# Optimization experiments

Hardware: AMD Instinct MI355X
Metric: run time of the kernel (lower is better)

## Reference

```python
import jax, jax.numpy as jnp
import numpy as np

B, T = 64, 500000

def setup_inputs() -> dict:
    key = jax.random.key(0)
    k1, k2 = jax.random.split(key)
    input_attenuation = jax.random.normal(k1, (B, T), dtype=jnp.float32)
    input_wet_dry = jax.random.randint(k2, (B, T), 0, 2).astype(jnp.bool_)
    return {"input_attenuation": input_attenuation, "input_wet_dry": input_wet_dry}

def reference(input_attenuation, input_wet_dry):
    # baseline[i] = baseline[i-1] if wet[i] else attenuation[i]; baseline[0] = attenuation[0].
    # Equivalent to gathering attenuation at the most recent 'dry' index (index 0 forced dry).
    Bn, Tn = input_attenuation.shape
    t = jnp.arange(Tn, dtype=jnp.int32)
    dry = jnp.logical_not(input_wet_dry).at[:, 0].set(True)  # timestep 0 always uses attenuation[0]
    pos = jnp.where(dry, t[None, :], jnp.int32(-1))          # [B, T]
    idx = jax.lax.associative_scan(jnp.maximum, pos, axis=1)  # running max = last dry index
    return jnp.take_along_axis(input_attenuation, idx, axis=1)
```

## Files before the change

### kernel.cpp

```cpp
#include <hip/hip_runtime.h>


constexpr int WSEG   = 4096;
constexpr int WCHUNK = 256;
constexpr int WITERS = WSEG / WCHUNK;

__global__ __launch_bounds__(256) void ffill_wave_kernel(
    const float* __restrict__ att,
    const int* __restrict__ wet,
    float* __restrict__ out,
    int T, int segsPerRow)
{
    const int lane = threadIdx.x & 63;
    const int wid  = threadIdx.x >> 6;
    const int s    = blockIdx.x * 4 + wid;
    if (s >= segsPerRow) return;
    const int r    = blockIdx.y;
    const long long rowBase = (long long)r * T;
    const int base = s * WSEG;

    float carry = 0.0f;
    int hi = base;
    while (hi > 0) {
        const int start = (hi >= 64) ? (hi - 64) : 0;
        const int idx   = start + lane;
        bool dry = false;
        if (idx < hi) dry = (wet[rowBase + idx] == 0) || (idx == 0);
        const unsigned long long m = __ballot(dry);
        if (m != 0ull) {
            const int src = 63 - __clzll(m);
            carry = att[rowBase + start + src];
            break;
        }
        hi = start;
    }

    int e = base + lane * 4;
    bool valid = (e < T);
    float4 a = make_float4(0.f, 0.f, 0.f, 0.f);
    int4  wv = make_int4(1, 1, 1, 1);
    if (valid) {
        a  = *reinterpret_cast<const float4*>(att + rowBase + e);
        wv = *reinterpret_cast<const int4*>(wet + rowBase + e);
    }

    for (int it = 0; it < WITERS; ++it) {
        float4 a_n = make_float4(0.f, 0.f, 0.f, 0.f);
        int4  wv_n = make_int4(1, 1, 1, 1);
        bool valid_n = false;
        if (it + 1 < WITERS) {
            const int en = e + WCHUNK;
            valid_n = (en < T);
            if (valid_n) {
                a_n  = *reinterpret_cast<const float4*>(att + rowBase + en);
                wv_n = *reinterpret_cast<const int4*>(wet + rowBase + en);
            }
        }

        bool d0 = (wv.x == 0) || (e == 0);
        bool d1 = (wv.y == 0);
        bool d2 = (wv.z == 0);
        bool d3 = (wv.w == 0);
        if (!valid) { d0 = d1 = d2 = d3 = false; }

        const bool has = d0 | d1 | d2 | d3;
        const float lastval = d3 ? a.w : (d2 ? a.z : (d1 ? a.y : a.x));

        const unsigned long long mask = __ballot(has);
        const unsigned long long pm = mask & ((1ull << lane) - 1ull);
        const int psrc = (pm != 0ull) ? (63 - __clzll(pm)) : 0;
        const float pval = __shfl(lastval, psrc);
        const float carry_in = (pm != 0ull) ? pval : carry;

        if (valid) {
            float running = carry_in;
            float4 o;
            running = d0 ? a.x : running;  o.x = running;
            running = d1 ? a.y : running;  o.y = running;
            running = d2 ? a.z : running;  o.z = running;
            running = d3 ? a.w : running;  o.w = running;
            *reinterpret_cast<float4*>(out + rowBase + e) = o;
        }

        const int wsrc = (mask != 0ull) ? (63 - __clzll(mask)) : 0;
        const float wval = __shfl(lastval, wsrc);
        if (mask != 0ull) carry = wval;

        a = a_n; wv = wv_n; valid = valid_n; e += WCHUNK;
    }
}

extern "C" void kernel_launch(void* const* d_in, const int* in_sizes, int n_in,
                              void* d_out, int out_size, void* d_ws, size_t ws_size,
                              hipStream_t stream) {
    const float* att = (const float*)d_in[0];
    const int* wet   = (const int*)d_in[1];
    float* out       = (float*)d_out;

    const int B = 64;
    const int T = in_sizes[0] / B;
    const int segsPerRow = (T + WSEG - 1) / WSEG;
    const int blocksX = (segsPerRow + 3) / 4;

    dim3 grid(blocksX, B);
    dim3 block(256);
    ffill_wave_kernel<<<grid, block, 0, stream>>>(att, wet, out, T, segsPerRow);
}
```

Before: 308.0 us.

## Batch-prefetch four chunks per iteration, enlarge segments, use nontemporal stores

The forward-fill loop now loads four 256-element chunks at once and prefetches the next batch of four, instead of one chunk ahead. This raises the number of memory requests in flight per wave. The segment length doubles to 8192, halving the redundant backward carry searches but also halving the number of waves. Outputs are written with nontemporal stores, and the carry is simplified to a shuffle from lane 63. The larger batches raise register pressure.

```diff
diff --git a/kernel.cpp b/kernel.cpp
--- a/kernel.cpp
+++ b/kernel.cpp
@@ -1,9 +1,13 @@
 #include <hip/hip_runtime.h>
 
 
-constexpr int WSEG   = 4096;
+constexpr int BATCH  = 4;
 constexpr int WCHUNK = 256;
-constexpr int WITERS = WSEG / WCHUNK;
+constexpr int OBLK   = BATCH * WCHUNK;
+constexpr int WSEG   = 8192;
+constexpr int OUTER  = WSEG / OBLK;
+
+typedef float f4v __attribute__((ext_vector_type(4)));
 
 __global__ __launch_bounds__(256) void ffill_wave_kernel(
     const float* __restrict__ att,
@@ -28,65 +32,80 @@
         if (idx < hi) dry = (wet[rowBase + idx] == 0) || (idx == 0);
         const unsigned long long m = __ballot(dry);
         if (m != 0ull) {
-            const int src = 63 - __clzll(m);
-            carry = att[rowBase + start + src];
+            carry = att[rowBase + start + (63 - __clzll(m))];
             break;
         }
         hi = start;
     }
 
-    int e = base + lane * 4;
-    bool valid = (e < T);
-    float4 a = make_float4(0.f, 0.f, 0.f, 0.f);
-    int4  wv = make_int4(1, 1, 1, 1);
-    if (valid) {
-        a  = *reinterpret_cast<const float4*>(att + rowBase + e);
-        wv = *reinterpret_cast<const int4*>(wet + rowBase + e);
+    float4 aC[BATCH]; int4 wC[BATCH];
+    const int e0 = base + lane * 4;
+    #pragma unroll
+    for (int k = 0; k < BATCH; ++k) {
+        const int e = e0 + k * WCHUNK;
+        if (e < T) {
+            aC[k] = *reinterpret_cast<const float4*>(att + rowBase + e);
+            wC[k] = *reinterpret_cast<const int4*>(wet + rowBase + e);
+        } else {
+            aC[k] = make_float4(0.f, 0.f, 0.f, 0.f);
+            wC[k] = make_int4(1, 1, 1, 1);
+        }
     }
 
-    for (int it = 0; it < WITERS; ++it) {
-        float4 a_n = make_float4(0.f, 0.f, 0.f, 0.f);
-        int4  wv_n = make_int4(1, 1, 1, 1);
-        bool valid_n = false;
-        if (it + 1 < WITERS) {
-            const int en = e + WCHUNK;
-            valid_n = (en < T);
-            if (valid_n) {
-                a_n  = *reinterpret_cast<const float4*>(att + rowBase + en);
-                wv_n = *reinterpret_cast<const int4*>(wet + rowBase + en);
+    for (int ot = 0; ot < OUTER; ++ot) {
+        float4 aN[BATCH]; int4 wN[BATCH];
+        #pragma unroll
+        for (int k = 0; k < BATCH; ++k) {
+            aN[k] = make_float4(0.f, 0.f, 0.f, 0.f);
+            wN[k] = make_int4(1, 1, 1, 1);
+        }
+        if (ot + 1 < OUTER) {
+            const int eb = e0 + (ot + 1) * OBLK;
+            #pragma unroll
+            for (int k = 0; k < BATCH; ++k) {
+                const int e = eb + k * WCHUNK;
+                if (e < T) {
+                    aN[k] = *reinterpret_cast<const float4*>(att + rowBase + e);
+                    wN[k] = *reinterpret_cast<const int4*>(wet + rowBase + e);
+                }
             }
         }
 
-        bool d0 = (wv.x == 0) || (e == 0);
-        bool d1 = (wv.y == 0);
-        bool d2 = (wv.z == 0);
-        bool d3 = (wv.w == 0);
-        if (!valid) { d0 = d1 = d2 = d3 = false; }
+        #pragma unroll
+        for (int k = 0; k < BATCH; ++k) {
+            const int e = e0 + ot * OBLK + k * WCHUNK;
+            const bool valid = (e < T);
 
-        const bool has = d0 | d1 | d2 | d3;
-        const float lastval = d3 ? a.w : (d2 ? a.z : (d1 ? a.y : a.x));
+            bool d0 = (wC[k].x == 0) || (e == 0);
+            bool d1 = (wC[k].y == 0);
+            bool d2 = (wC[k].z == 0);
+            bool d3 = (wC[k].w == 0);
+            if (!valid) { d0 = d1 = d2 = d3 = false; }
 
-        const unsigned long long mask = __ballot(has);
-        const unsigned long long pm = mask & ((1ull << lane) - 1ull);
-        const int psrc = (pm != 0ull) ? (63 - __clzll(pm)) : 0;
-        const float pval = __shfl(lastval, psrc);
-        const float carry_in = (pm != 0ull) ? pval : carry;
+            const bool has = d0 | d1 | d2 | d3;
+            const float lastval = d3 ? aC[k].w : (d2 ? aC[k].z : (d1 ? aC[k].y : aC[k].x));
 
-        if (valid) {
+            const unsigned long long mask = __ballot(has);
+            const unsigned long long pm = mask & ((1ull << lane) - 1ull);
+            const int psrc = (pm != 0ull) ? (63 - __clzll(pm)) : 0;
+            const float pval = __shfl(lastval, psrc);
+            const float carry_in = (pm != 0ull) ? pval : carry;
+
             float running = carry_in;
-            float4 o;
-            running = d0 ? a.x : running;  o.x = running;
-            running = d1 ? a.y : running;  o.y = running;
-            running = d2 ? a.z : running;  o.z = running;
-            running = d3 ? a.w : running;  o.w = running;
-            *reinterpret_cast<float4*>(out + rowBase + e) = o;
+            f4v o;
+            running = d0 ? aC[k].x : running;  o.x = running;
+            running = d1 ? aC[k].y : running;  o.y = running;
+            running = d2 ? aC[k].z : running;  o.z = running;
+            running = d3 ? aC[k].w : running;  o.w = running;
+            if (valid) {
+                __builtin_nontemporal_store(o, reinterpret_cast<f4v*>(out + rowBase + e));
+            }
+
+            carry = __shfl(running, 63);
         }
 
-        const int wsrc = (mask != 0ull) ? (63 - __clzll(mask)) : 0;
-        const float wval = __shfl(lastval, wsrc);
-        if (mask != 0ull) carry = wval;
-
-        a = a_n; wv = wv_n; valid = valid_n; e += WCHUNK;
+        #pragma unroll
+        for (int k = 0; k < BATCH; ++k) { aC[k] = aN[k]; wC[k] = wN[k]; }
     }
 }
 
```

Measured after the change: 312.7 us. No clear change (+1.5%).

## Use one wavefront per 256-element chunk with lookback and XCD block swizzle

Applied to the files above, without the earlier changes.

Each wavefront now handles a single 256-element chunk instead of looping over a 4096-element segment. This produces many more independent waves to hide memory latency. The carry is found by first checking a 64-element lookback window preloaded alongside the main loads, then falling back to a backward scan. Block indices are also remapped so consecutive chunks land on the same XCD. The trade-off is more redundant lookback reads and extra launch overhead per element.

```diff
diff --git a/kernel.cpp b/kernel.cpp
--- a/kernel.cpp
+++ b/kernel.cpp
@@ -1,92 +1,91 @@
 #include <hip/hip_runtime.h>
 
 
-constexpr int WSEG   = 4096;
-constexpr int WCHUNK = 256;
-constexpr int WITERS = WSEG / WCHUNK;
+constexpr int CHUNK = 256;
 
-__global__ __launch_bounds__(256) void ffill_wave_kernel(
+typedef float f4v __attribute__((ext_vector_type(4)));
+
+__global__ __launch_bounds__(256) void ffill_kernel(
     const float* __restrict__ att,
     const int* __restrict__ wet,
     float* __restrict__ out,
-    int T, int segsPerRow)
+    int T, int chunksPerRow)
 {
+    const int nwg = gridDim.x;
+    const int q   = nwg >> 3;
+    const int rr  = nwg & 7;
+    const int xcd = blockIdx.x & 7;
+    const int bix = blockIdx.x >> 3;
+    const int bswz = (xcd < rr ? xcd * (q + 1) : rr * (q + 1) + (xcd - rr) * q) + bix;
+
     const int lane = threadIdx.x & 63;
     const int wid  = threadIdx.x >> 6;
-    const int s    = blockIdx.x * 4 + wid;
-    if (s >= segsPerRow) return;
+    const int c    = bswz * 4 + wid;
+    if (c >= chunksPerRow) return;
     const int r    = blockIdx.y;
     const long long rowBase = (long long)r * T;
-    const int base = s * WSEG;
+    const int base = c * CHUNK;
+
+    float att_lb = 0.0f; int wet_lb = 1;
+    if (base > 0) {
+        const int i = base - 64 + lane;
+        att_lb = att[rowBase + i];
+        wet_lb = wet[rowBase + i];
+    }
+
+    const int e = base + lane * 4;
+    const bool valid = (e < T);
+    float4 a = make_float4(0.f, 0.f, 0.f, 0.f);
+    int4  w = make_int4(1, 1, 1, 1);
+    if (valid) {
+        a = *reinterpret_cast<const float4*>(att + rowBase + e);
+        w = *reinterpret_cast<const int4*>(wet + rowBase + e);
+    }
 
     float carry = 0.0f;
-    int hi = base;
-    while (hi > 0) {
-        const int start = (hi >= 64) ? (hi - 64) : 0;
-        const int idx   = start + lane;
-        bool dry = false;
-        if (idx < hi) dry = (wet[rowBase + idx] == 0) || (idx == 0);
-        const unsigned long long m = __ballot(dry);
+    if (base > 0) {
+        const unsigned long long m = __ballot(wet_lb == 0);
         if (m != 0ull) {
-            const int src = 63 - __clzll(m);
-            carry = att[rowBase + start + src];
-            break;
+            carry = __shfl(att_lb, 63 - __clzll(m));
+        } else {
+            int hi = base - 64;
+            while (hi > 0) {
+                const int start = (hi >= 64) ? (hi - 64) : 0;
+                const int idx   = start + lane;
+                const bool dry  = (idx < hi) && ((wet[rowBase + idx] == 0) || (idx == 0));
+                const unsigned long long mm = __ballot(dry);
+                if (mm != 0ull) {
+                    carry = att[rowBase + start + (63 - __clzll(mm))];
+                    break;
+                }
+                hi = start;
+            }
         }
-        hi = start;
     }
 
-    int e = base + lane * 4;
-    bool valid = (e < T);
-    float4 a = make_float4(0.f, 0.f, 0.f, 0.f);
-    int4  wv = make_int4(1, 1, 1, 1);
+    bool d0 = (w.x == 0) || (e == 0);
+    bool d1 = (w.y == 0);
+    bool d2 = (w.z == 0);
+    bool d3 = (w.w == 0);
+    if (!valid) { d0 = d1 = d2 = d3 = false; }
+
+    const bool has = d0 | d1 | d2 | d3;
+    const float lastval = d3 ? a.w : (d2 ? a.z : (d1 ? a.y : a.x));
+
+    const unsigned long long mask = __ballot(has);
+    const unsigned long long pm   = mask & ((1ull << lane) - 1ull);
+    const int   psrc = (pm != 0ull) ? (63 - __clzll(pm)) : 0;
+    const float pval = __shfl(lastval, psrc);
+    const float carry_in = (pm != 0ull) ? pval : carry;
+
     if (valid) {
-        a  = *reinterpret_cast<const float4*>(att + rowBase + e);
-        wv = *reinterpret_cast<const int4*>(wet + rowBase + e);
-    }
-
-    for (int it = 0; it < WITERS; ++it) {
-        float4 a_n = make_float4(0.f, 0.f, 0.f, 0.f);
-        int4  wv_n = make_int4(1, 1, 1, 1);
-        bool valid_n = false;
-        if (it + 1 < WITERS) {
-            const int en = e + WCHUNK;
-            valid_n = (en < T);
-            if (valid_n) {
-                a_n  = *reinterpret_cast<const float4*>(att + rowBase + en);
-                wv_n = *reinterpret_cast<const int4*>(wet + rowBase + en);
-            }
-        }
-
-        bool d0 = (wv.x == 0) || (e == 0);
-        bool d1 = (wv.y == 0);
-        bool d2 = (wv.z == 0);
-        bool d3 = (wv.w == 0);
-        if (!valid) { d0 = d1 = d2 = d3 = false; }
-
-        const bool has = d0 | d1 | d2 | d3;
-        const float lastval = d3 ? a.w : (d2 ? a.z : (d1 ? a.y : a.x));
-
-        const unsigned long long mask = __ballot(has);
-        const unsigned long long pm = mask & ((1ull << lane) - 1ull);
-        const int psrc = (pm != 0ull) ? (63 - __clzll(pm)) : 0;
-        const float pval = __shfl(lastval, psrc);
-        const float carry_in = (pm != 0ull) ? pval : carry;
-
-        if (valid) {
-            float running = carry_in;
-            float4 o;
-            running = d0 ? a.x : running;  o.x = running;
-            running = d1 ? a.y : running;  o.y = running;
-            running = d2 ? a.z : running;  o.z = running;
-            running = d3 ? a.w : running;  o.w = running;
-            *reinterpret_cast<float4*>(out + rowBase + e) = o;
-        }
-
-        const int wsrc = (mask != 0ull) ? (63 - __clzll(mask)) : 0;
-        const float wval = __shfl(lastval, wsrc);
-        if (mask != 0ull) carry = wval;
-
-        a = a_n; wv = wv_n; valid = valid_n; e += WCHUNK;
+        float running = carry_in;
+        f4v o;
+        running = d0 ? a.x : running;  o.x = running;
+        running = d1 ? a.y : running;  o.y = running;
+        running = d2 ? a.z : running;  o.z = running;
+        running = d3 ? a.w : running;  o.w = running;
+        *reinterpret_cast<f4v*>(out + rowBase + e) = o;
     }
 }
 
@@ -99,10 +98,10 @@
 
     const int B = 64;
     const int T = in_sizes[0] / B;
-    const int segsPerRow = (T + WSEG - 1) / WSEG;
-    const int blocksX = (segsPerRow + 3) / 4;
+    const int chunksPerRow = (T + CHUNK - 1) / CHUNK;
+    const int blocksX = (chunksPerRow + 3) / 4;
 
     dim3 grid(blocksX, B);
     dim3 block(256);
-    ffill_wave_kernel<<<grid, block, 0, stream>>>(att, wet, out, T, segsPerRow);
+    ffill_kernel<<<grid, block, 0, stream>>>(att, wet, out, T, chunksPerRow);
 }
```

New measurement: 294.3 us. -4.4%, faster.
